# Performance work log

Hardware: AMD Instinct MI355X
Metric: run time of the kernel (lower is better)

The kernel has to match this reference:

```python
import jax, jax.numpy as jnp
import numpy as np

D_MODEL = 256; N_HEADS = 8; D_FFN = 1024; N_LEVELS = 4; N_POINTS = 4
HEAD_DIM = D_MODEL // N_HEADS
SHAPES = ((100, 100), (50, 50), (25, 25), (13, 13))  # static (H, W) per level
LEN_V = sum(h * w for h, w in SHAPES)  # 13294
BS = 8; NQ = 900


def layer_norm(x, g, b, eps=1e-5):
    m = x.mean(-1, keepdims=True)
    v = ((x - m) ** 2).mean(-1, keepdims=True)
    return (x - m) * jax.lax.rsqrt(v + eps) * g + b


def bilinear_sample(val, loc, H, W):
    # val: [bs, nH, H*W, hd]; loc: [bs, nq, nH, P, 2] normalized to [0,1].
    # Matches torch grid_sample(bilinear, zeros padding, align_corners=False)
    # with grid = 2*loc - 1, i.e. pixel coords x = loc_x*W - 0.5.
    bs, nq, nH, P, _ = loc.shape
    x = loc[..., 0] * W - 0.5
    y = loc[..., 1] * H - 0.5
    x0 = jnp.floor(x); y0 = jnp.floor(y)
    fx = x - x0; fy = y - y0  # grads flow to loc through fx/fy
    x0 = x0.astype(jnp.int32); y0 = y0.astype(jnp.int32)
    out = jnp.zeros((bs, nq, nH, P, HEAD_DIM), val.dtype)
    for dy, wy in ((0, 1.0 - fy), (1, fy)):
        for dx, wx in ((0, 1.0 - fx), (1, fx)):
            xi = x0 + dx; yi = y0 + dy
            valid = (xi >= 0) & (xi < W) & (yi >= 0) & (yi < H)
            idx = jnp.clip(yi, 0, H - 1) * W + jnp.clip(xi, 0, W - 1)  # [bs,nq,nH,P]
            idx = idx.transpose(0, 2, 1, 3).reshape(bs, nH, nq * P)
            g = jnp.take_along_axis(val, idx[..., None], axis=2)  # [bs,nH,nq*P,hd]
            g = g.reshape(bs, nH, nq, P, HEAD_DIM).transpose(0, 2, 1, 3, 4)
            w = (wx * wy * valid).astype(val.dtype)[..., None]
            out = out + g * w
    return out  # [bs, nq, nH, P, hd]


def setup_inputs() -> dict:
    key = jax.random.key(0)
    ks = jax.random.split(key, 16)
    d = D_MODEL
    w = lambda k, shape: (jax.random.normal(k, shape) * 0.02).astype(jnp.float32)
    z = lambda n: jnp.zeros((n,), jnp.float32)
    o = lambda n: jnp.ones((n,), jnp.float32)
    return {
        "embed": jax.random.normal(ks[0], (BS, NQ, d), jnp.float32),
        "refer_bbox": jax.random.uniform(ks[1], (BS, NQ, 4), jnp.float32),  # cxcywh in [0,1]
        "feats": jax.random.normal(ks[2], (BS, LEN_V, d), jnp.float32),
        "query_pos": jax.random.normal(ks[3], (BS, NQ, d), jnp.float32),
        "Wq": w(ks[4], (d, d)), "bq": z(d), "Wk": w(ks[5], (d, d)), "bk": z(d),
        "Wv": w(ks[6], (d, d)), "bv": z(d), "Wo": w(ks[7], (d, d)), "bo": z(d),
        "g1": o(d), "b1": z(d),
        "Wval": w(ks[8], (d, d)), "bval": z(d),
        "Woff": w(ks[9], (d, N_HEADS * N_LEVELS * N_POINTS * 2)), "boff": z(N_HEADS * N_LEVELS * N_POINTS * 2),
        "Waw": w(ks[10], (d, N_HEADS * N_LEVELS * N_POINTS)), "baw": z(N_HEADS * N_LEVELS * N_POINTS),
        "Wop": w(ks[11], (d, d)), "bop": z(d),
        "g2": o(d), "b2": z(d),
        "W1": w(ks[12], (d, D_FFN)), "bf1": z(D_FFN),
        "W2": w(ks[13], (D_FFN, d)), "bf2": z(d),
        "g3": o(d), "b3": z(d),
    }


def reference(embed, refer_bbox, feats, query_pos, Wq, bq, Wk, bk, Wv, bv, Wo, bo,
              g1, b1, Wval, bval, Woff, boff, Waw, baw, Wop, bop, g2, b2,
              W1, bf1, W2, bf2, g3, b3):
    bs, nq, d = embed.shape
    # ---- self attention (q = k = embed + query_pos, v = embed) ----
    qk_in = embed + query_pos
    q = (qk_in @ Wq + bq).reshape(bs, nq, N_HEADS, HEAD_DIM)
    k = (qk_in @ Wk + bk).reshape(bs, nq, N_HEADS, HEAD_DIM)
    v = (embed @ Wv + bv).reshape(bs, nq, N_HEADS, HEAD_DIM)
    scores = jnp.einsum('bqhd,bkhd->bhqk', q, k) * (HEAD_DIM ** -0.5)
    attn = jax.nn.softmax(scores, -1)
    sa = jnp.einsum('bhqk,bkhd->bqhd', attn, v).reshape(bs, nq, d) @ Wo + bo
    embed = layer_norm(embed + sa, g1, b1)
    # ---- MSDeformAttn cross attention ----
    query = embed + query_pos
    rb = refer_bbox[:, :, None, :]  # [bs, nq, 1, 4] (refer_bbox.unsqueeze(2))
    value = (feats @ Wval + bval).reshape(bs, LEN_V, N_HEADS, HEAD_DIM)
    off = (query @ Woff + boff).reshape(bs, nq, N_HEADS, N_LEVELS, N_POINTS, 2)
    aw = jax.nn.softmax((query @ Waw + baw).reshape(bs, nq, N_HEADS, N_LEVELS * N_POINTS), -1)
    aw = aw.reshape(bs, nq, N_HEADS, N_LEVELS, N_POINTS)
    # num_points == 4 branch: loc = cxcy + off/P * wh * 0.5
    loc = rb[:, :, None, :, None, :2] + off / N_POINTS * rb[:, :, None, :, None, 2:] * 0.5
    out = jnp.zeros((bs, nq, N_HEADS, HEAD_DIM), embed.dtype)
    start = 0
    for l, (H, W) in enumerate(SHAPES):
        val_l = value[:, start:start + H * W].transpose(0, 2, 1, 3)  # [bs,nH,HW,hd]
        s = bilinear_sample(val_l, loc[:, :, :, l], H, W)  # [bs,nq,nH,P,hd]
        out = out + (s * aw[:, :, :, l, :, None]).sum(3)
        start += H * W
    ca = out.reshape(bs, nq, d) @ Wop + bop
    embed = layer_norm(embed + ca, g2, b2)
    # ---- FFN ----
    ff = jax.nn.relu(embed @ W1 + bf1) @ W2 + bf2
    return layer_norm(embed + ff, g3, b3)
```

## Files before the change

### kernel.cpp

```cpp
#include <hip/hip_runtime.h>
#include <hip/hip_bf16.h>
#include <cstddef>

#define BS 8
#define NQ 900
#define DM 256
#define LEN_V 13294

using bf16x8 = __attribute__((ext_vector_type(8))) __bf16;
using f32x4  = __attribute__((ext_vector_type(4))) float;

__device__ __forceinline__ unsigned short f2bf(float f) {
    union { float f; unsigned int u; } v; v.f = f;
    unsigned int r = v.u + 0x7FFFu + ((v.u >> 16) & 1u);
    return (unsigned short)(r >> 16);
}
__device__ __forceinline__ float bf2f(unsigned short u) {
    union { unsigned int u; float f; } v; v.u = ((unsigned int)u) << 16;
    return v.f;
}

#define SW(r) (((r) + ((r) >> 2)) & 3)

#define FLAG_RELU 1
#define FLAG_OBF  2
#define FLAG_SWAP 4
#define FLAG_QKV  8

#define AS1(p) ((const __attribute__((address_space(1))) void*)(p))
#define AS3(p) ((__attribute__((address_space(3))) void*)(p))

#define VMW6() do {                                        \
    __builtin_amdgcn_sched_barrier(0);                     \
    asm volatile("s_waitcnt vmcnt(6)" ::: "memory");       \
    __builtin_amdgcn_sched_barrier(0);                     \
} while (0)
#define VMW0() do {                                        \
    __builtin_amdgcn_sched_barrier(0);                     \
    asm volatile("s_waitcnt vmcnt(0)" ::: "memory");       \
    __builtin_amdgcn_sched_barrier(0);                     \
} while (0)

struct WDesc { const float* src; unsigned short* dst; int K; int N; float scale; };
struct WPrepArgs { WDesc w[10]; };

__global__ __launch_bounds__(256) void wprep_kernel(WPrepArgs args)
{
    WDesc d = args.w[blockIdx.z];
    int k0 = blockIdx.x * 32;
    int n0 = blockIdx.y * 32;
    if (k0 >= d.K || n0 >= d.N) return;
    __shared__ unsigned short t[32][33];
    int tx = threadIdx.x & 31, ty = threadIdx.x >> 5;
    #pragma unroll
    for (int i = 0; i < 4; ++i) {
        int kk = ty + i * 8;
        t[kk][tx] = f2bf(d.src[(size_t)(k0 + kk) * d.N + n0 + tx] * d.scale);
    }
    __syncthreads();
    #pragma unroll
    for (int i = 0; i < 4; ++i) {
        int nn = ty + i * 8;
        d.dst[(size_t)(n0 + nn) * d.K + k0 + tx] = t[tx][nn];
    }
}

__global__ __launch_bounds__(256) void bias_concat_kernel(
    const float* __restrict__ bq, const float* __restrict__ bk,
    const float* __restrict__ bv, const float* __restrict__ boff,
    const float* __restrict__ baw, float* __restrict__ bqkv,
    float* __restrict__ boffaw)
{
    const float sc = 0.17677669529663687f;
    int t = blockIdx.x * 256 + threadIdx.x;
    if (t < 256)       bqkv[t] = bq[t] * sc;
    else if (t < 512)  bqkv[t] = bk[t - 256];
    else if (t < 768)  bqkv[t] = bv[t - 512];
    if (t < 256)       boffaw[t] = boff[t];
    else if (t < 384)  boffaw[t] = baw[t - 256];
}

__global__ __launch_bounds__(256) void gemm_val(
    const float* __restrict__ A, const unsigned short* __restrict__ BT,
    const float* __restrict__ bias, unsigned short* __restrict__ C,
    int M, int N, int K)
{
    __shared__ uint4 SMEM[3072];

    const int tid = threadIdx.x;
    const int lane = tid & 63;
    const int wave = tid >> 6;
    const int wm = wave >> 1;
    const int wn = wave & 1;
    const int row0 = blockIdx.y * 128;
    const int col0 = blockIdx.x * 128;

    f32x4 acc[4][4];
    #pragma unroll
    for (int i = 0; i < 4; ++i)
        #pragma unroll
        for (int j = 0; j < 4; ++j)
            acc[i][j] = {0.f, 0.f, 0.f, 0.f};

    const int lr = lane & 15;
    const int lc = lane >> 4;

    const int achunk = (lane & 7) ^ ((lane >> 3) & 7);
    const int bchunk = (lane & 3) ^ ((lane >> 2) & 3);

    auto STAGE = [&](int k0, int buf) {
        uint4* Ab = SMEM + buf * 1536;
        uint4* Bb = Ab + 1024;
        #pragma unroll
        for (int c = 0; c < 4; ++c) {
            int r = wave * 32 + c * 8 + (lane >> 3);
            int gr = row0 + r; if (gr >= M) gr = M - 1;
            const float* g = A + (size_t)gr * K + k0 + achunk * 4;
            __builtin_amdgcn_global_load_lds(AS1(g), AS3(Ab + (wave * 4 + c) * 64), 16, 0, 0);
        }
        #pragma unroll
        for (int c = 0; c < 2; ++c) {
            int r = wave * 32 + c * 16 + (lane >> 2);
            const unsigned short* g = BT + (size_t)(col0 + r) * K + k0 + bchunk * 8;
            __builtin_amdgcn_global_load_lds(AS1(g), AS3(Bb + (wave * 2 + c) * 64), 16, 0, 0);
        }
    };

    auto MSTEP = [&](int buf) {
        const float* Af = (const float*)(SMEM + buf * 1536);
        const bf16x8* Bb8 = (const bf16x8*)(SMEM + buf * 1536 + 1024);
        bf16x8 af[4], bfr[4];
        #pragma unroll
        for (int mi = 0; mi < 4; ++mi) {
            int R = wm * 64 + mi * 16 + lr;
            int s0 = (2 * lc) ^ (R & 7);
            int s1 = (2 * lc + 1) ^ (R & 7);
            f32x4 a0 = *(const f32x4*)(Af + R * 32 + s0 * 4);
            f32x4 a1 = *(const f32x4*)(Af + R * 32 + s1 * 4);
            union { unsigned short us[8]; bf16x8 v; } u;
            u.us[0] = f2bf(a0[0]); u.us[1] = f2bf(a0[1]);
            u.us[2] = f2bf(a0[2]); u.us[3] = f2bf(a0[3]);
            u.us[4] = f2bf(a1[0]); u.us[5] = f2bf(a1[1]);
            u.us[6] = f2bf(a1[2]); u.us[7] = f2bf(a1[3]);
            af[mi] = u.v;
        }
        #pragma unroll
        for (int ni = 0; ni < 4; ++ni) {
            int R = wn * 64 + ni * 16 + lr;
            bfr[ni] = Bb8[R * 4 + (lc ^ (R & 3))];
        }
        #pragma unroll
        for (int mi = 0; mi < 4; ++mi)
            #pragma unroll
            for (int ni = 0; ni < 4; ++ni)
                acc[mi][ni] = __builtin_amdgcn_mfma_f32_16x16x32_bf16(
                    af[mi], bfr[ni], acc[mi][ni], 0, 0, 0);
    };

    const int NS = K >> 5;
    STAGE(0, 0);
    for (int s = 0; s < NS; s += 2) {
        STAGE((s + 1) * 32, 1);
        VMW6();
        __syncthreads();
        MSTEP(0);
        __syncthreads();
        if (s + 2 < NS) {
            STAGE((s + 2) * 32, 0);
            VMW6();
        } else {
            VMW0();
        }
        __syncthreads();
        MSTEP(1);
        __syncthreads();
    }
    VMW0();

    {
        unsigned short* RP = (unsigned short*)SMEM;
        float bval[4];
        #pragma unroll
        for (int ni = 0; ni < 4; ++ni) {
            int col = col0 + wn * 64 + ni * 16 + lr;
            bval[ni] = (col < N) ? bias[col] : 0.f;
        }
        #pragma unroll
        for (int h2 = 0; h2 < 2; ++h2) {
            __syncthreads();
            if (wm == h2) {
                #pragma unroll
                for (int ni = 0; ni < 4; ++ni) {
                    int colL = wn * 64 + ni * 16 + lr;
                    #pragma unroll
                    for (int mi = 0; mi < 4; ++mi) {
                        #pragma unroll
                        for (int rg = 0; rg < 4; ++rg) {
                            int rowL = mi * 16 + lc * 4 + rg;
                            RP[rowL * 136 + colL] = f2bf(acc[mi][ni][rg] + bval[ni]);
                        }
                    }
                }
            }
            __syncthreads();
            {
                int r = tid >> 2;
                int c = tid & 3;
                int grow = row0 + h2 * 64 + r;
                if (grow < M) {
                    #pragma unroll
                    for (int j = 0; j < 4; ++j) {
                        int gcol = col0 + c * 32 + j * 8;
                        uint4 vq = *(const uint4*)&RP[r * 136 + c * 32 + j * 8];
                        *(uint4*)(C + (size_t)grow * N + gcol) = vq;
                    }
                }
            }
        }
    }
}

#define SLOADA(B, k0) do {                                                    \
    if constexpr (ABF) {                                                      \
        const unsigned short* ap_ = Abf + (size_t)agr * K + (k0) + ah;        \
        qa##B = aok ? *(const uint4*)ap_ : z4;                                \
    } else {                                                                  \
        if (aok) {                                                            \
            const float* ap_ = Afp + (size_t)agr * K + (k0) + ah;             \
            pa##B##0 = *(const f32x4*)(ap_);                                  \
            pa##B##1 = *(const f32x4*)(ap_ + 4);                              \
            if (A2) {                                                         \
                const float* a2_ = A2 + (size_t)agr * K + (k0) + ah;          \
                pa##B##0 += *(const f32x4*)(a2_);                             \
                pa##B##1 += *(const f32x4*)(a2_ + 4);                         \
            }                                                                 \
        } else { pa##B##0 = zf4; pa##B##1 = zf4; }                            \
    }                                                                         \
    { const unsigned short* bp_ = BT + (size_t)bgr * K + (k0) + ah;           \
      pb##B = *(const uint4*)bp_; }                                           \
} while (0)

#define SSTAGE(B) do {                                                        \
    if constexpr (ABF) {                                                      \
        As4[ar * 4 + (ac ^ SW(ar))] = qa##B;                                  \
    } else {                                                                  \
        union { unsigned short us_[8]; uint4 q_; } u_;                        \
        u_.us_[0] = f2bf(pa##B##0[0]); u_.us_[1] = f2bf(pa##B##0[1]);         \
        u_.us_[2] = f2bf(pa##B##0[2]); u_.us_[3] = f2bf(pa##B##0[3]);         \
        u_.us_[4] = f2bf(pa##B##1[0]); u_.us_[5] = f2bf(pa##B##1[1]);         \
        u_.us_[6] = f2bf(pa##B##1[2]); u_.us_[7] = f2bf(pa##B##1[3]);         \
        As4[ar * 4 + (ac ^ SW(ar))] = u_.q_;                                  \
    }                                                                         \
    Bs4[ar * 4 + (ac ^ SW(ar))] = pb##B;                                      \
} while (0)

#define SMFMA() do {                                                          \
    bf16x8 af[2], bfr[2];                                                     \
    _Pragma("unroll")                                                         \
    for (int mi = 0; mi < 2; ++mi) {                                          \
        int r = wm * 32 + mi * 16 + lr;                                       \
        af[mi] = Asb[r * 4 + (lc ^ SW(r))];                                   \
    }                                                                         \
    _Pragma("unroll")                                                         \
    for (int ni = 0; ni < 2; ++ni) {                                          \
        int r = wn * 32 + ni * 16 + lr;                                       \
        bfr[ni] = Bsb[r * 4 + (lc ^ SW(r))];                                  \
    }                                                                         \
    _Pragma("unroll")                                                         \
    for (int mi = 0; mi < 2; ++mi)                                            \
        _Pragma("unroll")                                                     \
        for (int ni = 0; ni < 2; ++ni)                                        \
            acc[mi][ni] = __builtin_amdgcn_mfma_f32_16x16x32_bf16(            \
                af[mi], bfr[ni], acc[mi][ni], 0, 0, 0);                       \
} while (0)

template<int ABF>
__global__ __launch_bounds__(256) void gemm_small(
    const void* __restrict__ Ain, const float* __restrict__ A2,
    const unsigned short* __restrict__ BT, const float* __restrict__ bias,
    void* __restrict__ Cout, int M, int N, int K, int flags)
{
    __shared__ uint4 SMEM[512];
    uint4* As4 = SMEM;
    uint4* Bs4 = SMEM + 256;

    const int tid = threadIdx.x;
    const int lane = tid & 63;
    const int wave = tid >> 6;
    const int wm = wave >> 1;
    const int wn = wave & 1;
    const int row0 = (flags & FLAG_SWAP ? blockIdx.y : blockIdx.x) * 64;
    const int col0 = (flags & FLAG_SWAP ? blockIdx.x : blockIdx.y) * 64;
    if ((flags & FLAG_QKV) && col0 >= 512) A2 = nullptr;

    const float* Afp = (const float*)Ain;
    const unsigned short* Abf = (const unsigned short*)Ain;

    f32x4 acc[2][2];
    #pragma unroll
    for (int i = 0; i < 2; ++i)
        #pragma unroll
        for (int j = 0; j < 2; ++j)
            acc[i][j] = {0.f, 0.f, 0.f, 0.f};

    const int ar = tid >> 2;
    const int ac = tid & 3;
    const int ah = ac * 8;
    const int agr = row0 + ar;
    const bool aok = agr < M;
    const int bgr = col0 + ar;
    const int lr = lane & 15;
    const int lc = lane >> 4;

    const bf16x8* Asb = (const bf16x8*)As4;
    const bf16x8* Bsb = (const bf16x8*)Bs4;
    const uint4 z4 = {0u, 0u, 0u, 0u};
    const f32x4 zf4 = {0.f, 0.f, 0.f, 0.f};

    f32x4 pa00, pa01, pa10, pa11;
    uint4 qa0, qa1;
    uint4 pb0, pb1;

    const int nsteps = K >> 5;
    SLOADA(0, 0);
    for (int s = 0; s < nsteps; s += 2) {
        __syncthreads();
        SSTAGE(0);
        SLOADA(1, (s + 1 < nsteps ? (s + 1) * 32 : 0));
        __syncthreads();
        SMFMA();
        __syncthreads();
        SSTAGE(1);
        SLOADA(0, (s + 2 < nsteps ? (s + 2) * 32 : 0));
        __syncthreads();
        SMFMA();
    }

    const int relu = flags & FLAG_RELU;
    if (!(flags & FLAG_OBF)) {
        float* C = (float*)Cout;
        #pragma unroll
        for (int ni = 0; ni < 2; ++ni) {
            int col = col0 + wn * 32 + ni * 16 + lr;
            if (col >= N) continue;
            float bval = bias[col];
            #pragma unroll
            for (int mi = 0; mi < 2; ++mi) {
                #pragma unroll
                for (int rg = 0; rg < 4; ++rg) {
                    int row = row0 + wm * 32 + mi * 16 + lc * 4 + rg;
                    if (row < M) {
                        float o = acc[mi][ni][rg] + bval;
                        if (relu) o = fmaxf(o, 0.f);
                        C[(size_t)row * N + col] = o;
                    }
                }
            }
        }
    } else {
        unsigned short* RP = (unsigned short*)SMEM;
        unsigned short* C = (unsigned short*)Cout;
        float bval[2];
        #pragma unroll
        for (int ni = 0; ni < 2; ++ni) {
            int col = col0 + wn * 32 + ni * 16 + lr;
            bval[ni] = (col < N) ? bias[col] : 0.f;
        }
        #pragma unroll
        for (int h2 = 0; h2 < 2; ++h2) {
            __syncthreads();
            if (wm == h2) {
                #pragma unroll
                for (int ni = 0; ni < 2; ++ni) {
                    int colL = wn * 32 + ni * 16 + lr;
                    #pragma unroll
                    for (int mi = 0; mi < 2; ++mi) {
                        #pragma unroll
                        for (int rg = 0; rg < 4; ++rg) {
                            int rowL = mi * 16 + lc * 4 + rg;
                            float o = acc[mi][ni][rg] + bval[ni];
                            if (relu) o = fmaxf(o, 0.f);
                            RP[rowL * 72 + colL] = f2bf(o);
                        }
                    }
                }
            }
            __syncthreads();
            {
                int r = tid >> 3;
                int c = tid & 7;
                int grow = row0 + h2 * 32 + r;
                int gcol = col0 + c * 8;
                if (grow < M && gcol < N) {
                    uint4 vq = *(const uint4*)&RP[r * 72 + c * 8];
                    *(uint4*)(C + (size_t)grow * N + gcol) = vq;
                }
            }
        }
    }
}

#define QKVS 768
__global__ __launch_bounds__(256) void attn_mfma_kernel(
    const unsigned short* __restrict__ qkv, float* __restrict__ out)
{
    __shared__ uint4 Kls[64 * 4];
    __shared__ uint4 Vtls[32 * 8];

    const int tid = threadIdx.x;
    const int lane = tid & 63;
    const int wave = tid >> 6;
    const int qcol = lane & 15;
    const int g = lane >> 4;
    const int bh = blockIdx.x;
    const int h = bh & 7, b = bh >> 3;
    const int qg = blockIdx.y * 64 + wave * 16 + qcol;
    const int qc = qg < NQ ? qg : NQ - 1;

    bf16x8 qf = *(const bf16x8*)(qkv + ((size_t)(b * NQ + qc)) * QKVS + h * 32 + g * 8);

    float mrun = -3.0e38f, lrun = 0.f;
    f32x4 oacc[2];
    oacc[0] = {0.f, 0.f, 0.f, 0.f};
    oacc[1] = {0.f, 0.f, 0.f, 0.f};
    const f32x4 zacc = {0.f, 0.f, 0.f, 0.f};

    const int kidx = tid >> 2, kdc = tid & 3;
    const int vkp = tid >> 3, vdc = tid & 7;
    const bf16x8* Kb = (const bf16x8*)Kls;
    const bf16x8* Vb = (const bf16x8*)Vtls;
    unsigned int* V32 = (unsigned int*)Vtls;

    for (int jb = 0; jb < NQ; jb += 64) {
        __syncthreads();
        {
            int gk = jb + kidx;
            const uint4 z = {0u, 0u, 0u, 0u};
            uint4 kv = (gk < NQ)
                ? *(const uint4*)(qkv + ((size_t)(b * NQ + gk)) * QKVS + 256 + h * 32 + kdc * 8)
                : z;
            Kls[kidx * 4 + (kdc ^ ((kidx >> 1) & 3))] = kv;
        }
        {
            int k0g = jb + 2 * vkp;
            ushort4 a = {0, 0, 0, 0}, c = {0, 0, 0, 0};
            if (k0g < NQ)
                a = *(const ushort4*)(qkv + ((size_t)(b * NQ + k0g)) * QKVS + 512 + h * 32 + vdc * 4);
            if (k0g + 1 < NQ)
                c = *(const ushort4*)(qkv + ((size_t)(b * NQ + k0g + 1)) * QKVS + 512 + h * 32 + vdc * 4);
            unsigned int p0 = (unsigned int)a.x | ((unsigned int)c.x << 16);
            unsigned int p1 = (unsigned int)a.y | ((unsigned int)c.y << 16);
            unsigned int p2 = (unsigned int)a.z | ((unsigned int)c.z << 16);
            unsigned int p3 = (unsigned int)a.w | ((unsigned int)c.w << 16);
            int d0 = vdc * 4;
            V32[(d0+0) * 32 + ((vkp >> 2) ^ ((d0+0) & 7)) * 4 + (vkp & 3)] = p0;
            V32[(d0+1) * 32 + ((vkp >> 2) ^ ((d0+1) & 7)) * 4 + (vkp & 3)] = p1;
            V32[(d0+2) * 32 + ((vkp >> 2) ^ ((d0+2) & 7)) * 4 + (vkp & 3)] = p2;
            V32[(d0+3) * 32 + ((vkp >> 2) ^ ((d0+3) & 7)) * 4 + (vkp & 3)] = p3;
        }
        __syncthreads();

        f32x4 sacc[4];
        #pragma unroll
        for (int kt = 0; kt < 4; ++kt) {
            int key = kt * 16 + qcol;
            bf16x8 kf = Kb[key * 4 + (g ^ ((key >> 1) & 3))];
            sacc[kt] = __builtin_amdgcn_mfma_f32_16x16x32_bf16(kf, qf, zacc, 0, 0, 0);
        }
        if (jb + 64 > NQ) {
            #pragma unroll
            for (int kt = 0; kt < 4; ++kt)
                #pragma unroll
                for (int r = 0; r < 4; ++r)
                    if (jb + kt * 16 + 4 * g + r >= NQ) sacc[kt][r] = -3.0e38f;
        }

        float mloc = -3.0e38f;
        #pragma unroll
        for (int kt = 0; kt < 4; ++kt)
            #pragma unroll
            for (int r = 0; r < 4; ++r)
                mloc = fmaxf(mloc, sacc[kt][r]);
        mloc = fmaxf(mloc, __shfl_xor(mloc, 16));
        mloc = fmaxf(mloc, __shfl_xor(mloc, 32));
        float mnew = fmaxf(mrun, mloc);
        float corr = __expf(mrun - mnew);
        mrun = mnew;

        float lloc = 0.f;
        unsigned int pk2[4][2];
        #pragma unroll
        for (int kt = 0; kt < 4; ++kt) {
            float p0 = __expf(sacc[kt][0] - mnew);
            float p1 = __expf(sacc[kt][1] - mnew);
            float p2 = __expf(sacc[kt][2] - mnew);
            float p3 = __expf(sacc[kt][3] - mnew);
            lloc += p0 + p1 + p2 + p3;
            pk2[kt][0] = (unsigned int)f2bf(p0) | ((unsigned int)f2bf(p1) << 16);
            pk2[kt][1] = (unsigned int)f2bf(p2) | ((unsigned int)f2bf(p3) << 16);
        }
        lloc += __shfl_xor(lloc, 16);
        lloc += __shfl_xor(lloc, 32);
        lrun = lrun * corr + lloc;
        #pragma unroll
        for (int ni = 0; ni < 2; ++ni)
            #pragma unroll
            for (int r = 0; r < 4; ++r)
                oacc[ni][r] *= corr;

        const int s0 = qcol + 32 * (g & 1);
        const bool hi = (g >> 1) != 0;
        #pragma unroll
        for (int tp = 0; tp < 2; ++tp) {
            int A0 = (int)pk2[2 * tp][0], A1 = (int)pk2[2 * tp][1];
            int B0 = (int)pk2[2 * tp + 1][0], B1 = (int)pk2[2 * tp + 1][1];
            int a0 = __shfl(A0, s0),      a1 = __shfl(A1, s0);
            int b0 = __shfl(B0, s0),      b1 = __shfl(B1, s0);
            int a2 = __shfl(A0, s0 + 16), a3 = __shfl(A1, s0 + 16);
            int b2 = __shfl(B0, s0 + 16), b3 = __shfl(B1, s0 + 16);
            union { unsigned int u[4]; bf16x8 v8; } pf;
            pf.u[0] = hi ? (unsigned int)b0 : (unsigned int)a0;
            pf.u[1] = hi ? (unsigned int)b1 : (unsigned int)a1;
            pf.u[2] = hi ? (unsigned int)b2 : (unsigned int)a2;
            pf.u[3] = hi ? (unsigned int)b3 : (unsigned int)a3;
            #pragma unroll
            for (int ni = 0; ni < 2; ++ni) {
                int d = ni * 16 + qcol;
                bf16x8 vf = Vb[d * 8 + ((4 * tp + g) ^ (d & 7))];
                oacc[ni] = __builtin_amdgcn_mfma_f32_16x16x32_bf16(vf, pf.v8, oacc[ni], 0, 0, 0);
            }
        }
    }

    if (qg < NQ) {
        float inv = 1.f / lrun;
        float* op = out + ((size_t)(b * NQ + qg)) * DM + h * 32;
        float4 o0, o1;
        o0.x = oacc[0][0] * inv; o0.y = oacc[0][1] * inv;
        o0.z = oacc[0][2] * inv; o0.w = oacc[0][3] * inv;
        o1.x = oacc[1][0] * inv; o1.y = oacc[1][1] * inv;
        o1.z = oacc[1][2] * inv; o1.w = oacc[1][3] * inv;
        *(float4*)(op + 4 * g) = o0;
        *(float4*)(op + 16 + 4 * g) = o1;
    }
}

__global__ __launch_bounds__(256) void deform_kernel(
    const unsigned short* __restrict__ value, const float* __restrict__ offaw,
    const float* __restrict__ rbbox, float* __restrict__ dout)
{
    int t = blockIdx.x * 256 + threadIdx.x;
    if (t >= BS * NQ * 64) return;
    int c = t & 7;
    int h = (t >> 3) & 7;
    int bq = t >> 6;
    int b = bq / NQ;

    const int Hs[4]     = {100, 50, 25, 13};
    const int Wsz[4]    = {100, 50, 25, 13};
    const int Starts[4] = {0, 10000, 12500, 13125};

    float4 rb = *(const float4*)(rbbox + (size_t)bq * 4);
    const float* offp = offaw + (size_t)bq * 384 + h * 32;
    const float* awp  = offaw + (size_t)bq * 384 + 256 + h * 16;
    const unsigned short* vb = value + ((size_t)b * LEN_V) * 256 + h * 32 + c * 4;

    float awv[16];
    #pragma unroll
    for (int i = 0; i < 4; ++i) {
        float4 f = *(const float4*)(awp + i * 4);
        awv[4*i+0] = f.x; awv[4*i+1] = f.y; awv[4*i+2] = f.z; awv[4*i+3] = f.w;
    }
    float mx = awv[0];
    #pragma unroll
    for (int i = 1; i < 16; ++i) mx = fmaxf(mx, awv[i]);
    float ssum = 0.f;
    #pragma unroll
    for (int i = 0; i < 16; ++i) { awv[i] = __expf(awv[i] - mx); ssum += awv[i]; }
    float sinv = 1.f / ssum;

    float4 acc = make_float4(0.f, 0.f, 0.f, 0.f);
    #pragma unroll
    for (int l = 0; l < 4; ++l) {
        const int H = Hs[l], W = Wsz[l], st = Starts[l];
        #pragma unroll
        for (int p = 0; p < 4; ++p) {
            float ox = offp[l * 8 + p * 2 + 0];
            float oy = offp[l * 8 + p * 2 + 1];
            float a_w = awv[l * 4 + p] * sinv;
            float xx = (rb.x + ox * 0.125f * rb.z) * W - 0.5f;
            float yy = (rb.y + oy * 0.125f * rb.w) * H - 0.5f;
            float x0f = floorf(xx), y0f = floorf(yy);
            float fx = xx - x0f, fy = yy - y0f;
            int x0 = (int)x0f, y0 = (int)y0f;
            #pragma unroll
            for (int dy = 0; dy < 2; ++dy) {
                int yi = y0 + dy;
                float wy = dy ? fy : (1.f - fy);
                bool vy = (yi >= 0) && (yi < H);
                int yc = min(max(yi, 0), H - 1);
                #pragma unroll
                for (int dx = 0; dx < 2; ++dx) {
                    int xi = x0 + dx;
                    float wx = dx ? fx : (1.f - fx);
                    bool vx = (xi >= 0) && (xi < W);
                    int xc = min(max(xi, 0), W - 1);
                    float wgt = a_w * wy * wx * ((vx && vy) ? 1.f : 0.f);
                    ushort4 gv = *(const ushort4*)(vb + (size_t)(st + yc * W + xc) * 256);
                    acc.x += wgt * bf2f(gv.x); acc.y += wgt * bf2f(gv.y);
                    acc.z += wgt * bf2f(gv.z); acc.w += wgt * bf2f(gv.w);
                }
            }
        }
    }
    *(float4*)(dout + (size_t)bq * 256 + h * 32 + c * 4) = acc;
}

__global__ __launch_bounds__(256) void ln_kernel(
    const float* __restrict__ x, const float* __restrict__ dx,
    const float* __restrict__ g, const float* __restrict__ bt,
    float* __restrict__ out, int rows)
{
    int row = blockIdx.x * 4 + (threadIdx.x >> 6);
    if (row >= rows) return;
    int lane = threadIdx.x & 63;
    size_t base = (size_t)row * 256 + lane * 4;
    float4 xv = *(const float4*)(x + base);
    float4 dv = *(const float4*)(dx + base);
    float a0 = xv.x + dv.x, a1 = xv.y + dv.y, a2 = xv.z + dv.z, a3 = xv.w + dv.w;
    float s = a0 + a1 + a2 + a3;
    float s2 = a0 * a0 + a1 * a1 + a2 * a2 + a3 * a3;
    #pragma unroll
    for (int o = 32; o; o >>= 1) {
        s += __shfl_xor(s, o);
        s2 += __shfl_xor(s2, o);
    }
    float mean = s * (1.f / 256.f);
    float var = s2 * (1.f / 256.f) - mean * mean;
    float inv = rsqrtf(var + 1e-5f);
    float4 gv = *(const float4*)(g + lane * 4);
    float4 bv = *(const float4*)(bt + lane * 4);
    float4 r;
    r.x = (a0 - mean) * inv * gv.x + bv.x;
    r.y = (a1 - mean) * inv * gv.y + bv.y;
    r.z = (a2 - mean) * inv * gv.z + bv.z;
    r.w = (a3 - mean) * inv * gv.w + bv.w;
    *(float4*)(out + base) = r;
}

extern "C" void kernel_launch(void* const* d_in, const int* in_sizes, int n_in,
                              void* d_out, int out_size, void* d_ws, size_t ws_size,
                              hipStream_t stream)
{
    const float* embed = (const float*)d_in[0];
    const float* rbbox = (const float*)d_in[1];
    const float* feats = (const float*)d_in[2];
    const float* qpos  = (const float*)d_in[3];
    const float* Wq = (const float*)d_in[4];  const float* bq = (const float*)d_in[5];
    const float* Wk = (const float*)d_in[6];  const float* bk = (const float*)d_in[7];
    const float* Wv = (const float*)d_in[8];  const float* bv = (const float*)d_in[9];
    const float* Wo = (const float*)d_in[10]; const float* bo = (const float*)d_in[11];
    const float* g1 = (const float*)d_in[12]; const float* b1 = (const float*)d_in[13];
    const float* Wval = (const float*)d_in[14]; const float* bval = (const float*)d_in[15];
    const float* Woff = (const float*)d_in[16]; const float* boff = (const float*)d_in[17];
    const float* Waw  = (const float*)d_in[18]; const float* baw  = (const float*)d_in[19];
    const float* Wop  = (const float*)d_in[20]; const float* bop  = (const float*)d_in[21];
    const float* g2 = (const float*)d_in[22]; const float* b2 = (const float*)d_in[23];
    const float* W1 = (const float*)d_in[24]; const float* bf1 = (const float*)d_in[25];
    const float* W2 = (const float*)d_in[26]; const float* bf2 = (const float*)d_in[27];
    const float* g3 = (const float*)d_in[28]; const float* b3 = (const float*)d_in[29];

    const int M = BS * NQ;
    const int MV = BS * LEN_V;
    const size_t E = (size_t)M * DM;
    const size_t VAL = (size_t)MV * DM;

    float* ws = (float*)d_ws;
    float* valueb = ws;
    float* qkvreg = ws + VAL;
    float* attb   = qkvreg + 3 * E;
    float* e1b    = attb + E;
    unsigned short* wbase = (unsigned short*)(e1b + E);
    unsigned short* wqkv_t   = wbase;
    unsigned short* wo_t     = wbase + 196608;
    unsigned short* wval_t   = wbase + 262144;
    unsigned short* woffaw_t = wbase + 327680;
    unsigned short* wop_t    = wbase + 425984;
    unsigned short* w1_t     = wbase + 491520;
    unsigned short* w2_t     = wbase + 753664;
    float* bqkv   = (float*)(wbase + 1015808);
    float* boffaw = bqkv + 768;

    unsigned short* valuebf = (unsigned short*)valueb;
    unsigned short* qkvbf   = (unsigned short*)qkvreg;
    float* sab    = qkvreg;
    float* offawb = qkvreg + E;
    float* doutb  = attb;
    float* cab    = qkvreg;
    float* e2b    = qkvreg + 2 * E;
    unsigned short* ffhb = (unsigned short*)valueb;
    float* ffb    = attb;

    dim3 blk(256);
    auto gsS = [](int m, int n) { return dim3((n + 63) / 64, (m + 63) / 64); };

    {
        const float sc = 0.17677669529663687f;
        WPrepArgs a;
        a.w[0] = {Wq,   wqkv_t,                 256, 256,  sc};
        a.w[1] = {Wk,   wqkv_t + 256 * 256,     256, 256,  1.f};
        a.w[2] = {Wv,   wqkv_t + 512 * 256,     256, 256,  1.f};
        a.w[3] = {Wo,   wo_t,                   256, 256,  1.f};
        a.w[4] = {Wval, wval_t,                 256, 256,  1.f};
        a.w[5] = {Woff, woffaw_t,               256, 256,  1.f};
        a.w[6] = {Waw,  woffaw_t + 256 * 256,   256, 128,  1.f};
        a.w[7] = {Wop,  wop_t,                  256, 256,  1.f};
        a.w[8] = {W1,   w1_t,                   256, 1024, 1.f};
        a.w[9] = {W2,   w2_t,                   1024, 256, 1.f};
        wprep_kernel<<<dim3(32, 32, 10), blk, 0, stream>>>(a);
        bias_concat_kernel<<<dim3(3), blk, 0, stream>>>(bq, bk, bv, boff, baw, bqkv, boffaw);
    }

    gemm_small<0><<<gsS(M, 768), blk, 0, stream>>>(embed, qpos, wqkv_t, bqkv, qkvbf, M, 768, 256, FLAG_SWAP | FLAG_QKV | FLAG_OBF);
    attn_mfma_kernel<<<dim3(BS * 8, (NQ + 63) / 64), blk, 0, stream>>>(qkvbf, attb);
    gemm_small<0><<<gsS(M, 256), blk, 0, stream>>>(attb, nullptr, wo_t, bo, sab, M, 256, 256, FLAG_SWAP);
    ln_kernel<<<dim3((M + 3) / 4), blk, 0, stream>>>(embed, sab, g1, b1, e1b, M);
    gemm_val<<<dim3(2, (MV + 127) / 128), blk, 0, stream>>>(feats, wval_t, bval, valuebf, MV, 256, 256);
    gemm_small<0><<<gsS(M, 384), blk, 0, stream>>>(e1b, qpos, woffaw_t, boffaw, offawb, M, 384, 256, FLAG_SWAP);
    deform_kernel<<<dim3((BS * NQ * 64 + 255) / 256), blk, 0, stream>>>(valuebf, offawb, rbbox, doutb);
    gemm_small<0><<<gsS(M, 256), blk, 0, stream>>>(doutb, nullptr, wop_t, bop, cab, M, 256, 256, FLAG_SWAP);
    ln_kernel<<<dim3((M + 3) / 4), blk, 0, stream>>>(e1b, cab, g2, b2, e2b, M);
    gemm_small<0><<<gsS(M, 1024), blk, 0, stream>>>(e2b, nullptr, w1_t, bf1, ffhb, M, 1024, 256, FLAG_SWAP | FLAG_RELU | FLAG_OBF);
    gemm_small<1><<<gsS(M, 256), blk, 0, stream>>>(ffhb, nullptr, w2_t, bf2, ffb, M, 256, 1024, FLAG_SWAP);
    ln_kernel<<<dim3((M + 3) / 4), blk, 0, stream>>>(e2b, ffb, g3, b3, (float*)d_out, M);
}
```

Measured before the change: 243.0 us.

## Rewrite value-projection GEMM with 512 threads and register-staged bf16 LDS tiles

Replaces the double-buffered global_load_lds value GEMM with a single-buffered version using 512 threads (8 waves, 2x4 wave grid). A tiles are converted from fp32 to bf16 in registers before the LDS store, which halves LDS footprint and avoids per-MFMA-step conversion. The LDS requirement drops sharply, which could raise occupancy. The cost is losing the async load/compute overlap: each k-step now issues global loads and then waits on them before two barriers.

```diff
diff --git a/kernel.cpp b/kernel.cpp
--- a/kernel.cpp
+++ b/kernel.cpp
@@ -26,20 +26,6 @@
 #define FLAG_OBF  2
 #define FLAG_SWAP 4
 #define FLAG_QKV  8
-
-#define AS1(p) ((const __attribute__((address_space(1))) void*)(p))
-#define AS3(p) ((__attribute__((address_space(3))) void*)(p))
-
-#define VMW6() do {                                        \
-    __builtin_amdgcn_sched_barrier(0);                     \
-    asm volatile("s_waitcnt vmcnt(6)" ::: "memory");       \
-    __builtin_amdgcn_sched_barrier(0);                     \
-} while (0)
-#define VMW0() do {                                        \
-    __builtin_amdgcn_sched_barrier(0);                     \
-    asm volatile("s_waitcnt vmcnt(0)" ::: "memory");       \
-    __builtin_amdgcn_sched_barrier(0);                     \
-} while (0)
 
 struct WDesc { const float* src; unsigned short* dst; int K; int N; float scale; };
 struct WPrepArgs { WDesc w[10]; };
@@ -80,109 +66,84 @@
     else if (t < 384)  boffaw[t] = baw[t - 256];
 }
 
-__global__ __launch_bounds__(256) void gemm_val(
+__global__ __launch_bounds__(512) void gemm_val2(
     const float* __restrict__ A, const unsigned short* __restrict__ BT,
     const float* __restrict__ bias, unsigned short* __restrict__ C,
     int M, int N, int K)
 {
-    __shared__ uint4 SMEM[3072];
+    __shared__ uint4 SMEM[1088];
+    uint4* As4 = SMEM;
+    uint4* Bs4 = SMEM + 512;
 
     const int tid = threadIdx.x;
     const int lane = tid & 63;
     const int wave = tid >> 6;
-    const int wm = wave >> 1;
-    const int wn = wave & 1;
+    const int wm = wave >> 2;
+    const int wn = wave & 3;
     const int row0 = blockIdx.y * 128;
     const int col0 = blockIdx.x * 128;
 
-    f32x4 acc[4][4];
+    f32x4 acc[4][2];
     #pragma unroll
     for (int i = 0; i < 4; ++i)
         #pragma unroll
-        for (int j = 0; j < 4; ++j)
+        for (int j = 0; j < 2; ++j)
             acc[i][j] = {0.f, 0.f, 0.f, 0.f};
 
+    const int sr = tid >> 2;
+    const int sc = tid & 3;
+    const int agr0 = row0 + sr;
+    const int agr = agr0 < M ? agr0 : M - 1;
+    const int bgr = col0 + sr;
     const int lr = lane & 15;
     const int lc = lane >> 4;
 
-    const int achunk = (lane & 7) ^ ((lane >> 3) & 7);
-    const int bchunk = (lane & 3) ^ ((lane >> 2) & 3);
-
-    auto STAGE = [&](int k0, int buf) {
-        uint4* Ab = SMEM + buf * 1536;
-        uint4* Bb = Ab + 1024;
-        #pragma unroll
-        for (int c = 0; c < 4; ++c) {
-            int r = wave * 32 + c * 8 + (lane >> 3);
-            int gr = row0 + r; if (gr >= M) gr = M - 1;
-            const float* g = A + (size_t)gr * K + k0 + achunk * 4;
-            __builtin_amdgcn_global_load_lds(AS1(g), AS3(Ab + (wave * 4 + c) * 64), 16, 0, 0);
-        }
-        #pragma unroll
-        for (int c = 0; c < 2; ++c) {
-            int r = wave * 32 + c * 16 + (lane >> 2);
-            const unsigned short* g = BT + (size_t)(col0 + r) * K + k0 + bchunk * 8;
-            __builtin_amdgcn_global_load_lds(AS1(g), AS3(Bb + (wave * 2 + c) * 64), 16, 0, 0);
-        }
-    };
-
-    auto MSTEP = [&](int buf) {
-        const float* Af = (const float*)(SMEM + buf * 1536);
-        const bf16x8* Bb8 = (const bf16x8*)(SMEM + buf * 1536 + 1024);
-        bf16x8 af[4], bfr[4];
-        #pragma unroll
-        for (int mi = 0; mi < 4; ++mi) {
-            int R = wm * 64 + mi * 16 + lr;
-            int s0 = (2 * lc) ^ (R & 7);
-            int s1 = (2 * lc + 1) ^ (R & 7);
-            f32x4 a0 = *(const f32x4*)(Af + R * 32 + s0 * 4);
-            f32x4 a1 = *(const f32x4*)(Af + R * 32 + s1 * 4);
-            union { unsigned short us[8]; bf16x8 v; } u;
+    const bf16x8* Asb = (const bf16x8*)As4;
+    const bf16x8* Bsb = (const bf16x8*)Bs4;
+
+    for (int k0 = 0; k0 < K; k0 += 32) {
+        const float* ap = A + (size_t)agr * K + k0 + sc * 8;
+        f32x4 a0 = *(const f32x4*)ap;
+        f32x4 a1 = *(const f32x4*)(ap + 4);
+        uint4 bq = *(const uint4*)(BT + (size_t)bgr * K + k0 + sc * 8);
+
+        __syncthreads();
+        {
+            union { unsigned short us[8]; uint4 q; } u;
             u.us[0] = f2bf(a0[0]); u.us[1] = f2bf(a0[1]);
             u.us[2] = f2bf(a0[2]); u.us[3] = f2bf(a0[3]);
             u.us[4] = f2bf(a1[0]); u.us[5] = f2bf(a1[1]);
             u.us[6] = f2bf(a1[2]); u.us[7] = f2bf(a1[3]);
-            af[mi] = u.v;
-        }
-        #pragma unroll
-        for (int ni = 0; ni < 4; ++ni) {
-            int R = wn * 64 + ni * 16 + lr;
-            bfr[ni] = Bb8[R * 4 + (lc ^ (R & 3))];
+            As4[sr * 4 + (sc ^ SW(sr))] = u.q;
+        }
+        Bs4[sr * 4 + (sc ^ SW(sr))] = bq;
+        __syncthreads();
+
+        bf16x8 af[4], bfr[2];
+        #pragma unroll
+        for (int mi = 0; mi < 4; ++mi) {
+            int r = wm * 64 + mi * 16 + lr;
+            af[mi] = Asb[r * 4 + (lc ^ SW(r))];
+        }
+        #pragma unroll
+        for (int ni = 0; ni < 2; ++ni) {
+            int r = wn * 32 + ni * 16 + lr;
+            bfr[ni] = Bsb[r * 4 + (lc ^ SW(r))];
         }
         #pragma unroll
         for (int mi = 0; mi < 4; ++mi)
             #pragma unroll
-            for (int ni = 0; ni < 4; ++ni)
+            for (int ni = 0; ni < 2; ++ni)
                 acc[mi][ni] = __builtin_amdgcn_mfma_f32_16x16x32_bf16(
                     af[mi], bfr[ni], acc[mi][ni], 0, 0, 0);
-    };
-
-    const int NS = K >> 5;
-    STAGE(0, 0);
-    for (int s = 0; s < NS; s += 2) {
-        STAGE((s + 1) * 32, 1);
-        VMW6();
-        __syncthreads();
-        MSTEP(0);
-        __syncthreads();
-        if (s + 2 < NS) {
-            STAGE((s + 2) * 32, 0);
-            VMW6();
-        } else {
-            VMW0();
-        }
-        __syncthreads();
-        MSTEP(1);
-        __syncthreads();
-    }
-    VMW0();
+    }
 
     {
         unsigned short* RP = (unsigned short*)SMEM;
-        float bval[4];
-        #pragma unroll
-        for (int ni = 0; ni < 4; ++ni) {
-            int col = col0 + wn * 64 + ni * 16 + lr;
+        float bval[2];
+        #pragma unroll
+        for (int ni = 0; ni < 2; ++ni) {
+            int col = col0 + wn * 32 + ni * 16 + lr;
             bval[ni] = (col < N) ? bias[col] : 0.f;
         }
         #pragma unroll
@@ -190,8 +151,8 @@
             __syncthreads();
             if (wm == h2) {
                 #pragma unroll
-                for (int ni = 0; ni < 4; ++ni) {
-                    int colL = wn * 64 + ni * 16 + lr;
+                for (int ni = 0; ni < 2; ++ni) {
+                    int colL = wn * 32 + ni * 16 + lr;
                     #pragma unroll
                     for (int mi = 0; mi < 4; ++mi) {
                         #pragma unroll
@@ -204,14 +165,15 @@
             }
             __syncthreads();
             {
-                int r = tid >> 2;
-                int c = tid & 3;
+                int r = tid >> 3;
+                int c = tid & 7;
                 int grow = row0 + h2 * 64 + r;
                 if (grow < M) {
                     #pragma unroll
-                    for (int j = 0; j < 4; ++j) {
-                        int gcol = col0 + c * 32 + j * 8;
-                        uint4 vq = *(const uint4*)&RP[r * 136 + c * 32 + j * 8];
+                    for (int j = 0; j < 2; ++j) {
+                        int cc = c * 2 + j;
+                        int gcol = col0 + cc * 8;
+                        uint4 vq = *(const uint4*)&RP[r * 136 + cc * 8];
                         *(uint4*)(C + (size_t)grow * N + gcol) = vq;
                     }
                 }
@@ -725,7 +687,7 @@
     attn_mfma_kernel<<<dim3(BS * 8, (NQ + 63) / 64), blk, 0, stream>>>(qkvbf, attb);
     gemm_small<0><<<gsS(M, 256), blk, 0, stream>>>(attb, nullptr, wo_t, bo, sab, M, 256, 256, FLAG_SWAP);
     ln_kernel<<<dim3((M + 3) / 4), blk, 0, stream>>>(embed, sab, g1, b1, e1b, M);
-    gemm_val<<<dim3(2, (MV + 127) / 128), blk, 0, stream>>>(feats, wval_t, bval, valuebf, MV, 256, 256);
+    gemm_val2<<<dim3(2, (MV + 127) / 128), dim3(512), 0, stream>>>(feats, wval_t, bval, valuebf, MV, 256, 256);
     gemm_small<0><<<gsS(M, 384), blk, 0, stream>>>(e1b, qpos, woffaw_t, boffaw, offawb, M, 384, 256, FLAG_SWAP);
     deform_kernel<<<dim3((BS * NQ * 64 + 255) / 256), blk, 0, stream>>>(valuebf, offawb, rbbox, doutb);
     gemm_small<0><<<gsS(M, 256), blk, 0, stream>>>(doutb, nullptr, wop_t, bop, cab, M, 256, 256, FLAG_SWAP);
```

After: 234.3 us. 3.6% less time.
